# Performance work log

Measured on AMD Instinct MI355X. Metric: run time of the kernel, lower is better.

The kernel has to match this reference:

```python
import jax, jax.numpy as jnp
import numpy as np

N, E = 4096, 40960
NODE_DIM, RADIAL_DIM = 16, 8
M, HD, LAT = 64, 32, 128
NUM_LAYERS = 2
R_MAX, POLY_P, ENV_NORM = 5.0, 6.0, 5.0
ISQRTD = 5.0  # math.isqrt(32) == 5 in the original source


def setup_inputs() -> dict:
    key = jax.random.key(0)
    ks = jax.random.split(key, 20)
    def w(k, shape, fan_in):
        return jax.random.normal(k, shape, jnp.float32) / np.float32(np.sqrt(fan_in))
    return {
        "node_attrs": jax.random.uniform(ks[0], (N, NODE_DIM), jnp.float32),
        "edge_radial": jax.random.normal(ks[1], (E, RADIAL_DIM), jnp.float32),
        "edge_angular": jax.random.normal(ks[2], (E, 4), jnp.float32),
        "edge_lengths": jax.random.uniform(ks[3], (E,), jnp.float32) * (R_MAX * 0.9),
        "edge_index": jax.random.randint(ks[4], (2, E), 0, N),
        "W_lat0": w(ks[5], (2 * NODE_DIM + RADIAL_DIM, LAT), 2 * NODE_DIM + RADIAL_DIM),
        "W_lat1": w(ks[6], (LAT + 2 * M, LAT), LAT + 2 * M),
        "W_final": w(ks[7], (LAT + 2 * M, M), LAT + 2 * M),
        "W_env0": w(ks[8], (LAT, 5 * M), LAT),  # 320 = feat weights(128) + env weights(128) + gate(64)
        "W_env1": w(ks[9], (LAT, 3 * M), LAT),  # 192 = env weights(128) + gate(64)
        "W_q": w(ks[10], (NUM_LAYERS, NODE_DIM, M * HD), NODE_DIM),
        "W_k": w(ks[11], (NUM_LAYERS, M, M * HD), M),
        "W_envlin": w(ks[12], (NUM_LAYERS, 2, M, M), M),
        "W_prod": w(ks[13], (NUM_LAYERS, NODE_DIM, M), NODE_DIM),
        "W_lin_s": w(ks[14], (NUM_LAYERS, 2, M, M), 2 * M),
        "W_lin_v": w(ks[15], (NUM_LAYERS, 3, M, M), 3 * M),
        "alpha": jax.random.normal(ks[16], (NUM_LAYERS,), jnp.float32),
    }


def _poly_cutoff(r):
    # PolynomialCutoff with p=6
    x = r / R_MAX
    p = POLY_P
    c = (1.0 - ((p + 1.0) * (p + 2.0) / 2.0) * x ** p
         + p * (p + 2.0) * x ** (p + 1.0)
         - (p * (p + 1.0) / 2.0) * x ** (p + 2.0))
    return jnp.where(x < 1.0, c, 0.0)


def reference(node_attrs, edge_radial, edge_angular, edge_lengths, edge_index,
              W_lat0, W_lat1, W_final, W_env0, W_env1, W_q, W_k,
              W_envlin, W_prod, W_lin_s, W_lin_v, alpha):
    n_nodes = node_attrs.shape[0]
    center, neigh = edge_index[0], edge_index[1]
    cutoff = _poly_cutoff(edge_lengths)[:, None]  # [E,1]
    sh0 = edge_angular[:, 0:1]                    # [E,1] l=0 SH
    sh1 = edge_angular[:, 1:4]                    # [E,3] l=1 SH

    # two-body latent
    two_body_in = jnp.concatenate([node_attrs[center], node_attrs[neigh], edge_radial], -1)
    latent = jax.nn.silu(two_body_in @ W_lat0) * cutoff  # [E,LAT]

    feat_s = feat_v = None
    for l in range(NUM_LAYERS):
        if l == 0:
            wts = latent @ W_env0
            w_feat = wts[:, :2 * M].reshape(-1, M, 2)
            w_env = wts[:, 2 * M:4 * M].reshape(-1, M, 2)
            w_gate = wts[:, 4 * M:]
            feat_s = w_feat[..., 0] * sh0                         # [E,M]
            feat_v = w_feat[..., 1][..., None] * sh1[:, None, :]  # [E,M,3]
        else:
            wts = latent @ W_env1
            w_env = wts[:, :2 * M].reshape(-1, M, 2)
            w_gate = wts[:, 2 * M:]
        # weighted-channel env embedding of the edge spherical harmonics
        emb_s = w_env[..., 0] * sh0                               # [E,M]
        emb_v = w_env[..., 1][..., None] * sh1[:, None, :]        # [E,M,3]
        # attention-like query/key scalar product per channel
        q = (node_attrs @ W_q[l]).reshape(-1, M, HD)[center]      # [E,M,HD]
        k = ((emb_s * w_gate) @ W_k[l]).reshape(-1, M, HD)        # [E,M,HD]
        attn = jax.nn.sigmoid(jnp.einsum('emd,emd->em', q, k) / ISQRTD)
        g_edge = attn * cutoff                                    # [E,M]
        # neighbor scatter-sum, normalized (env_sum_normalizations buffer = 5.0)
        env_s = jax.ops.segment_sum(emb_s * g_edge, center, num_segments=n_nodes) / ENV_NORM
        env_v = jax.ops.segment_sum(emb_v * g_edge[..., None], center, num_segments=n_nodes) / ENV_NORM
        # env_linear: per-l channel mixing
        env_s = env_s @ W_envlin[l, 0]
        env_v = jnp.einsum('nmc,mk->nkc', env_v, W_envlin[l, 1])
        # element-dependent product-basis gating (simplified EquivariantProductBasisBlock)
        gate_n = node_attrs @ W_prod[l]
        env_s = env_s * gate_n
        env_v = env_v * gate_n[..., None]
        es, ev = env_s[center], env_v[center]
        # channel-wise (uuu) tensor product at lmax=1
        s1 = feat_s * es                                             # 0e x 0e -> 0e
        s2 = jnp.einsum('emc,emc->em', feat_v, ev) / jnp.sqrt(3.0)   # 1o x 1o -> 0e
        v1 = feat_s[..., None] * ev                                  # 0e x 1o -> 1o
        v2 = feat_v * es[..., None]                                  # 1o x 0e -> 1o
        v3 = jnp.cross(feat_v, ev) / jnp.sqrt(2.0)                   # 1o x 1o -> 1o
        scalars = jnp.stack([s1, s2], 1)       # [E,2,M]
        vectors = jnp.stack([v1, v2, v3], 1)   # [E,3,M,3]
        # irreps Linear: path + channel mixing
        feat_s = jnp.einsum('epm,pmk->ek', scalars, W_lin_s[l]) / jnp.sqrt(2.0 * M)
        feat_v = jnp.einsum('epmc,pmk->ekc', vectors, W_lin_v[l]) / jnp.sqrt(3.0 * M)
        sc_flat = scalars.transpose(0, 2, 1).reshape(-1, 2 * M)  # tp scalar outs
        lat_in = jnp.concatenate([latent, sc_flat], -1)
        if l < NUM_LAYERS - 1:
            new_lat = jax.nn.silu(lat_in @ W_lat1) * cutoff
            co = 1.0 / jnp.sqrt(1.0 + alpha[l] ** 2)  # latent resnet update
            latent = co * latent + (alpha[l] * co) * new_lat
        else:
            feat_s = lat_in @ W_final  # final_latent -> out scalar features [E,M]
    # reshape_back_features: concat scalar + vector irrep blocks
    return jnp.concatenate([feat_s, feat_v.reshape(-1, 3 * M)], -1)  # [E, 4*M]
```

## Files before the change

### kernel.cpp

```cpp
#include <hip/hip_runtime.h>

constexpr int Nn  = 4096;
constexpr int Ee  = 40960;
constexpr int ND  = 16;
constexpr int Mm  = 64;
constexpr int HD  = 32;

#define DI __device__ __forceinline__

DI float silu_f(float x) { return x / (1.f + __expf(-x)); }
DI unsigned short bf16r(float f) {
    unsigned u = __float_as_uint(f);
    return (unsigned short)((u + 0x7FFFu + ((u >> 16) & 1u)) >> 16);
}
DI float bf16f(unsigned short h) { return __uint_as_float(((unsigned)h) << 16); }

__global__ void k_zero(float* __restrict__ p, int n) {
    int i = blockIdx.x * 256 + threadIdx.x;
    if (i < n) p[i] = 0.f;
}

__global__ void k_cutoff(const float* __restrict__ len, float* __restrict__ cut) {
    int e = blockIdx.x * 256 + threadIdx.x;
    if (e >= Ee) return;
    float x  = len[e] * 0.2f;
    float x2 = x * x, x4 = x2 * x2, x6 = x4 * x2;
    float c  = 1.f - 28.f * x6 + 48.f * x6 * x - 21.f * x4 * x4;
    cut[e] = (x < 1.f) ? c : 0.f;
}

__global__ void k_qk(const float* __restrict__ Wq, const float* __restrict__ Wk,
                     float* __restrict__ QKT) {
    int idx = blockIdx.x * 256 + threadIdx.x;
    int mp = idx & 63;
    int m  = (idx >> 6) & 63;
    int a  = (idx >> 12) & 15;
    int l  = idx >> 16;
    const float* q = Wq + ((size_t)(l * ND + a)) * 2048 + m * HD;
    const float* k = Wk + ((size_t)(l * Mm + mp)) * 2048 + m * HD;
    float acc = 0.f;
#pragma unroll
    for (int d = 0; d < HD; ++d) acc += q[d] * k[d];
    QKT[(((size_t)l * 16 + a) * 16 + (mp >> 2)) * 256 + m * 4 + (mp & 3)] = acc;
}

__global__ void k_permB(const float* __restrict__ Wls, float* __restrict__ Bp) {
    int idx = blockIdx.x * 256 + threadIdx.x;
    int k = idx & 63, row = idx >> 6;
    int m = row >> 1, pp = row & 1;
    Bp[row * 64 + k] = Wls[pp * 4096 + m * 64 + k];
}

__global__ void k_qw(const float* __restrict__ na, const float* __restrict__ QKT,
                     ushort4* __restrict__ QWh) {
    int n = blockIdx.x >> 2;
    int g = ((blockIdx.x & 3) << 2) + (threadIdx.x >> 6);
    int m = threadIdx.x & 63;
    const float4* QK4 = (const float4*)QKT;
    const float* nar = na + n * ND;
    float4 acc = {0.f, 0.f, 0.f, 0.f};
#pragma unroll
    for (int a = 0; a < ND; ++a) {
        float w = nar[a];
        float4 q = QK4[(a * 16 + g) * 64 + m];
        acc.x += w * q.x; acc.y += w * q.y; acc.z += w * q.z; acc.w += w * q.w;
    }
    ushort4 o;
    o.x = bf16r(acc.x); o.y = bf16r(acc.y); o.z = bf16r(acc.z); o.w = bf16r(acc.w);
    QWh[((size_t)n * 16 + g) * 64 + m] = o;
}

__global__ void k_A2(const float* __restrict__ wts, const float* __restrict__ ang,
                     const float* __restrict__ cut, const int* __restrict__ ctr,
                     const ushort4* __restrict__ QWh,
                     float* __restrict__ env_s, float* __restrict__ env_v) {
    __shared__ float xs[256];
    int wid = threadIdx.x >> 6, m = threadIdx.x & 63;
    int e = blockIdx.x * 4 + wid;
    int c = ctr[e];
    float cute = cut[e];
    float4 sh = ((const float4*)ang)[e];
    const float* w = wts + (size_t)e * 192;
    float2 we = ((const float2*)w)[m];
    float wg = w[128 + m];
    float es_ = we.x * sh.x;
    float ev0 = we.y * sh.y, ev1 = we.y * sh.z, ev2 = we.y * sh.w;
    xs[threadIdx.x] = es_ * wg;
    __syncthreads();
    const float4* xv = (const float4*)(xs + wid * 64);
    const ushort4* qrow = QWh + (size_t)c * 1024;
    float logit = 0.f;
#pragma unroll
    for (int g = 0; g < 16; ++g) {
        ushort4 q = qrow[g * 64 + m];
        float4 x = xv[g];
        logit += bf16f(q.x) * x.x + bf16f(q.y) * x.y + bf16f(q.z) * x.z + bf16f(q.w) * x.w;
    }
    float attn = 1.f / (1.f + __expf(-logit * 0.2f));
    float ga = attn * cute * 0.2f;
    atomicAdd(&env_s[(size_t)c * 64 + m], es_ * ga);
    atomicAdd(&env_v[(size_t)c * 192 + m],       ev0 * ga);
    atomicAdd(&env_v[(size_t)c * 192 + 64 + m],  ev1 * ga);
    atomicAdd(&env_v[(size_t)c * 192 + 128 + m], ev2 * ga);
}

__global__ void k_C_s(const float* __restrict__ fs, const float* __restrict__ fv,
                      const float* __restrict__ es_t, const float* __restrict__ ev_t,
                      const int* __restrict__ ctr, float* __restrict__ sc_mp) {
    int wid = threadIdx.x >> 6, m = threadIdx.x & 63;
    int e = blockIdx.x * 4 + wid;
    int c = ctr[e];
    float es  = es_t[(size_t)c * 64 + m];
    float ev0 = ev_t[(size_t)c * 192 + m];
    float ev1 = ev_t[(size_t)c * 192 + 64 + m];
    float ev2 = ev_t[(size_t)c * 192 + 128 + m];
    float f  = fs[(size_t)e * 64 + m];
    float g0 = fv[(size_t)e * 192 + m];
    float g1 = fv[(size_t)e * 192 + 64 + m];
    float g2 = fv[(size_t)e * 192 + 128 + m];
    float2 sp;
    sp.x = f * es;
    sp.y = (g0 * ev0 + g1 * ev1 + g2 * ev2) * 0.5773502691896258f;
    ((float2*)sc_mp)[(size_t)e * 64 + m] = sp;
}

template <int P>
__global__ void k_C_v(const float* __restrict__ fs, const float* __restrict__ fv,
                      const float* __restrict__ es_t, const float* __restrict__ ev_t,
                      const int* __restrict__ ctr, float* __restrict__ vec) {
    constexpr int Pb = (P + 1) % 3, Pc = (P + 2) % 3;
    int wid = threadIdx.x >> 6, m = threadIdx.x & 63;
    int e = blockIdx.x * 4 + wid;
    int c = ctr[e];
    float es  = es_t[(size_t)c * 64 + m];
    float evP = ev_t[(size_t)c * 192 + P  * 64 + m];
    float evB = ev_t[(size_t)c * 192 + Pb * 64 + m];
    float evC = ev_t[(size_t)c * 192 + Pc * 64 + m];
    float f   = fs[(size_t)e * 64 + m];
    float gP  = fv[(size_t)e * 192 + P  * 64 + m];
    float gB  = fv[(size_t)e * 192 + Pb * 64 + m];
    float gC  = fv[(size_t)e * 192 + Pc * 64 + m];
    constexpr float is2 = 0.7071067811865475f;
    vec[(size_t)e * 192 + m]       = f * evP;
    vec[(size_t)e * 192 + 64 + m]  = gP * es;
    vec[(size_t)e * 192 + 128 + m] = (gB * evC - gC * evB) * is2;
}

__global__ __launch_bounds__(256) void k_gemm(
    const float* __restrict__ A, int lda, const float* __restrict__ A2,
    const int* __restrict__ ctr, const int* __restrict__ ngh,
    const float* __restrict__ naw, const float* __restrict__ er,
    const float* __restrict__ B, int ldb, int K,
    float* __restrict__ C, int ldc, int cstride, float scale,
    const float* __restrict__ cut, const float* __restrict__ oldlat,
    const float* __restrict__ alphap, const float* __restrict__ gate,
    const float* __restrict__ ang, float* __restrict__ fsP, float* __restrict__ fvP,
    int modeA, int modeE) {
    __shared__ float a_s[16][72];
    __shared__ float b_s[16][64];
    int t = threadIdx.x;
    int row0 = blockIdx.x * 64;
    int j0 = blockIdx.y * 64;
    int tx = t & 15, ty = t >> 4;
    int ar = t & 63, akq = t >> 6;
    int bj = (t & 15) * 4, bk = t >> 4;
    float acc[4][4] = {};
    int nchunks = (K + 15) >> 4;
    for (int ch = 0; ch < nchunks; ++ch) {
        int k0 = ch * 16;
        {
            int row = row0 + ar;
            int k = k0 + akq * 4;
            float4 v;
            if (modeA == 0) {
                v = *(const float4*)(A + (size_t)row * lda + k);
            } else if (modeA == 1) {
                const float* src = (k < 128) ? (A + (size_t)row * 128 + k)
                                             : (A2 + (size_t)row * 128 + (k - 128));
                v = *(const float4*)src;
            } else {
                float tmp[4];
#pragma unroll
                for (int i = 0; i < 4; ++i) {
                    int kk = k + i; float val = 0.f;
                    if (kk < 16)      val = naw[(size_t)ctr[row] * 16 + kk];
                    else if (kk < 32) val = naw[(size_t)ngh[row] * 16 + (kk - 16)];
                    else if (kk < 40) val = er[(size_t)row * 8 + (kk - 32)];
                    tmp[i] = val;
                }
                v.x = tmp[0]; v.y = tmp[1]; v.z = tmp[2]; v.w = tmp[3];
            }
            a_s[akq * 4 + 0][ar] = v.x;
            a_s[akq * 4 + 1][ar] = v.y;
            a_s[akq * 4 + 2][ar] = v.z;
            a_s[akq * 4 + 3][ar] = v.w;
        }
        {
            int k = k0 + bk;
            float4 v = {0.f, 0.f, 0.f, 0.f};
            if (k < K) v = *(const float4*)(B + (size_t)k * ldb + j0 + bj);
            *(float4*)&b_s[bk][bj] = v;
        }
        __syncthreads();
#pragma unroll
        for (int k = 0; k < 16; ++k) {
            float4 a4 = *(const float4*)&a_s[k][ty * 4];
            float4 b4 = *(const float4*)&b_s[k][tx * 4];
            acc[0][0] += a4.x * b4.x; acc[0][1] += a4.x * b4.y; acc[0][2] += a4.x * b4.z; acc[0][3] += a4.x * b4.w;
            acc[1][0] += a4.y * b4.x; acc[1][1] += a4.y * b4.y; acc[1][2] += a4.y * b4.z; acc[1][3] += a4.y * b4.w;
            acc[2][0] += a4.z * b4.x; acc[2][1] += a4.z * b4.y; acc[2][2] += a4.z * b4.z; acc[2][3] += a4.z * b4.w;
            acc[3][0] += a4.w * b4.x; acc[3][1] += a4.w * b4.y; acc[3][2] += a4.w * b4.z; acc[3][3] += a4.w * b4.w;
        }
        __syncthreads();
    }
    float a0 = 0.f, co = 1.f;
    if (modeE == 2) { a0 = alphap[0]; co = rsqrtf(1.f + a0 * a0); }
#pragma unroll
    for (int r = 0; r < 4; ++r) {
        int row = row0 + ty * 4 + r;
        if (modeE == 4) {
            float4 sh = ((const float4*)ang)[row];
#pragma unroll
            for (int i = 0; i < 4; ++i) {
                int col = j0 + tx * 4 + i;
                int m = col >> 1;
                float v = acc[r][i];
                if (col & 1) {
                    fvP[(size_t)row * 192 + m]       = v * sh.y;
                    fvP[(size_t)row * 192 + 64 + m]  = v * sh.z;
                    fvP[(size_t)row * 192 + 128 + m] = v * sh.w;
                } else {
                    fsP[(size_t)row * 64 + m] = v * sh.x;
                }
            }
            continue;
        }
        float cu = (modeE == 1 || modeE == 2) ? cut[row] : 0.f;
#pragma unroll
        for (int i = 0; i < 4; ++i) {
            int col = j0 + tx * 4 + i;
            float v;
            if (modeE == 1)      v = silu_f(acc[r][i]) * cu;
            else if (modeE == 2) {
                float nl = silu_f(acc[r][i]) * cu;
                v = co * oldlat[(size_t)row * 128 + col] + a0 * co * nl;
            } else if (modeE == 3) v = acc[r][i] * scale * gate[(size_t)row * 64 + col];
            else                 v = acc[r][i] * scale;
            C[(size_t)row * ldc + (size_t)col * cstride] = v;
        }
    }
}

extern "C" void kernel_launch(void* const* d_in, const int* in_sizes, int n_in,
                              void* d_out, int out_size, void* d_ws, size_t ws_size,
                              hipStream_t stream) {
    const float* na     = (const float*)d_in[0];
    const float* er     = (const float*)d_in[1];
    const float* ang    = (const float*)d_in[2];
    const float* len    = (const float*)d_in[3];
    const int*   ei     = (const int*)d_in[4];
    const float* W_lat0 = (const float*)d_in[5];
    const float* W_lat1 = (const float*)d_in[6];
    const float* W_fin  = (const float*)d_in[7];
    const float* W_env0 = (const float*)d_in[8];
    const float* W_env1 = (const float*)d_in[9];
    const float* W_q    = (const float*)d_in[10];
    const float* W_k    = (const float*)d_in[11];
    const float* W_evl  = (const float*)d_in[12];
    const float* W_prod = (const float*)d_in[13];
    const float* W_ls   = (const float*)d_in[14];
    const float* W_lv   = (const float*)d_in[15];
    const float* alpha  = (const float*)d_in[16];
    float* out = (float*)d_out;

    const int* ctr = ei;
    const int* ngh = ei + Ee;

    float* ws = (float*)d_ws;
    float* wtsv  = ws;
    float* QWreg = wtsv + 7864320;
    float* sc_mp = QWreg;
    float* fvB   = QWreg + 8388608;
    float* lat   = QWreg + 16777216;
    float* lat2  = lat + 5242880;
    float* fs    = lat2 + 5242880;
    float* cut   = fs + 2621440;
    float* QKT   = cut + 40960;
    float* env_s = QKT + 131072;
    float* env_v = env_s + 262144;
    float* es_t  = env_v + 786432;
    float* ev_t  = es_t + 262144;
    float* gateb = ev_t + 786432;
    float* Wlsp  = gateb + 262144;
    float* fvA   = out;

    const float rs128 = 0.08838834764831845f;
    const float rs192 = 0.07216878364870323f;

    k_cutoff<<<(Ee + 255) / 256, 256, 0, stream>>>(len, cut);
    k_qk<<<512, 256, 0, stream>>>(W_q, W_k, QKT);
    k_permB<<<32, 256, 0, stream>>>(W_ls, Wlsp);
    k_gemm<<<dim3(Ee / 64, 2), 256, 0, stream>>>(nullptr, 0, nullptr, ctr, ngh, na, er,
        W_lat0, 128, 40, lat, 128, 1, 1.f, cut, nullptr, nullptr, nullptr, nullptr, nullptr, nullptr, 2, 1);

    for (int l = 0; l < 2; ++l) {
        const float* latin = (l == 0) ? lat : lat2;
        k_qw<<<Nn * 4, 256, 0, stream>>>(na, QKT + (size_t)l * 65536, (ushort4*)QWreg);
        k_zero<<<(Nn * 256 + 255) / 256, 256, 0, stream>>>(env_s, Nn * 256);
        if (l == 0) {
            k_gemm<<<dim3(Ee / 64, 2), 256, 0, stream>>>(latin, 128, nullptr, nullptr, nullptr, nullptr, nullptr,
                W_env0, 320, 128, nullptr, 0, 1, 1.f, nullptr, nullptr, nullptr, nullptr, ang, fs, fvA, 0, 4);
            k_gemm<<<dim3(Ee / 64, 3), 256, 0, stream>>>(latin, 128, nullptr, nullptr, nullptr, nullptr, nullptr,
                W_env0 + 128, 320, 128, wtsv, 192, 1, 1.f, nullptr, nullptr, nullptr, nullptr, nullptr, nullptr, nullptr, 0, 0);
        } else {
            k_gemm<<<dim3(Ee / 64, 3), 256, 0, stream>>>(latin, 128, nullptr, nullptr, nullptr, nullptr, nullptr,
                W_env1, 192, 128, wtsv, 192, 1, 1.f, nullptr, nullptr, nullptr, nullptr, nullptr, nullptr, nullptr, 0, 0);
        }
        k_A2<<<Ee / 4, 256, 0, stream>>>(wtsv, ang, cut, ctr, (const ushort4*)QWreg, env_s, env_v);
        k_gemm<<<dim3(Nn / 64, 1), 256, 0, stream>>>(na, 16, nullptr, nullptr, nullptr, nullptr, nullptr,
            W_prod + (size_t)l * 1024, 64, 16, gateb, 64, 1, 1.f, nullptr, nullptr, nullptr, nullptr, nullptr, nullptr, nullptr, 0, 0);
        k_gemm<<<dim3(Nn / 64, 1), 256, 0, stream>>>(env_s, 64, nullptr, nullptr, nullptr, nullptr, nullptr,
            W_evl + (size_t)l * 8192, 64, 64, es_t, 64, 1, 1.f, nullptr, nullptr, nullptr, gateb, nullptr, nullptr, nullptr, 0, 3);
        for (int c = 0; c < 3; ++c)
            k_gemm<<<dim3(Nn / 64, 1), 256, 0, stream>>>(env_v + c * 64, 192, nullptr, nullptr, nullptr, nullptr, nullptr,
                W_evl + (size_t)l * 8192 + 4096, 64, 64, ev_t + c * 64, 192, 1, 1.f, nullptr, nullptr, nullptr, gateb, nullptr, nullptr, nullptr, 0, 3);
        const float* fvsrc = (l == 0) ? fvA : fvB;
        k_C_s<<<Ee / 4, 256, 0, stream>>>(fs, fvsrc, es_t, ev_t, ctr, sc_mp);
        for (int c = 0; c < 3; ++c) {
            if (c == 0)      k_C_v<0><<<Ee / 4, 256, 0, stream>>>(fs, fvsrc, es_t, ev_t, ctr, wtsv);
            else if (c == 1) k_C_v<1><<<Ee / 4, 256, 0, stream>>>(fs, fvsrc, es_t, ev_t, ctr, wtsv);
            else             k_C_v<2><<<Ee / 4, 256, 0, stream>>>(fs, fvsrc, es_t, ev_t, ctr, wtsv);
            if (l == 0) {
                k_gemm<<<dim3(Ee / 64, 1), 256, 0, stream>>>(wtsv, 192, nullptr, nullptr, nullptr, nullptr, nullptr,
                    W_lv, 64, 192, fvB + c * 64, 192, 1, rs192, nullptr, nullptr, nullptr, nullptr, nullptr, nullptr, nullptr, 0, 0);
            } else {
                k_gemm<<<dim3(Ee / 64, 1), 256, 0, stream>>>(wtsv, 192, nullptr, nullptr, nullptr, nullptr, nullptr,
                    W_lv + 12288, 64, 192, out + 64 + c, 256, 3, rs192, nullptr, nullptr, nullptr, nullptr, nullptr, nullptr, nullptr, 0, 0);
            }
        }
        if (l == 0) {
            k_gemm<<<dim3(Ee / 64, 1), 256, 0, stream>>>(sc_mp, 128, nullptr, nullptr, nullptr, nullptr, nullptr,
                Wlsp, 64, 128, fs, 64, 1, rs128, nullptr, nullptr, nullptr, nullptr, nullptr, nullptr, nullptr, 0, 0);
            k_gemm<<<dim3(Ee / 64, 2), 256, 0, stream>>>(lat, 128, sc_mp, nullptr, nullptr, nullptr, nullptr,
                W_lat1, 128, 256, lat2, 128, 1, 1.f, cut, lat, alpha, nullptr, nullptr, nullptr, nullptr, 1, 2);
        } else {
            k_gemm<<<dim3(Ee / 64, 1), 256, 0, stream>>>(lat2, 128, sc_mp, nullptr, nullptr, nullptr, nullptr,
                W_fin, 64, 256, out, 256, 1, 1.f, nullptr, nullptr, nullptr, nullptr, nullptr, nullptr, nullptr, 1, 0);
        }
    }
    (void)in_sizes; (void)n_in; (void)out_size; (void)ws_size;
}
```

Before: 895.1 us.

## Enlarge GEMM tile to 128 rows with 128 threads and fold k_C_s into k_C_v

The generic GEMM kernel now uses a 128x64 output tile computed by 128 threads, each holding a 2x4x2x4 register block, which raises register-level reuse of the shared-memory operands. All launches are updated to the new grid and block size. Separately, the scalar tensor-product kernel k_C_s is removed and its work is done inside k_C_v<0>, which already loads the same operands, saving one launch and a redundant gather. In exchange the GEMM uses more registers per thread and launches half as many blocks, and the node GEMMs (4096 rows) get only 32 blocks, which may leave the GPU underoccupied.

```diff
diff --git a/kernel.cpp b/kernel.cpp
--- a/kernel.cpp
+++ b/kernel.cpp
@@ -104,30 +104,11 @@
     atomicAdd(&env_v[(size_t)c * 192 + 128 + m], ev2 * ga);
 }
 
-__global__ void k_C_s(const float* __restrict__ fs, const float* __restrict__ fv,
-                      const float* __restrict__ es_t, const float* __restrict__ ev_t,
-                      const int* __restrict__ ctr, float* __restrict__ sc_mp) {
-    int wid = threadIdx.x >> 6, m = threadIdx.x & 63;
-    int e = blockIdx.x * 4 + wid;
-    int c = ctr[e];
-    float es  = es_t[(size_t)c * 64 + m];
-    float ev0 = ev_t[(size_t)c * 192 + m];
-    float ev1 = ev_t[(size_t)c * 192 + 64 + m];
-    float ev2 = ev_t[(size_t)c * 192 + 128 + m];
-    float f  = fs[(size_t)e * 64 + m];
-    float g0 = fv[(size_t)e * 192 + m];
-    float g1 = fv[(size_t)e * 192 + 64 + m];
-    float g2 = fv[(size_t)e * 192 + 128 + m];
-    float2 sp;
-    sp.x = f * es;
-    sp.y = (g0 * ev0 + g1 * ev1 + g2 * ev2) * 0.5773502691896258f;
-    ((float2*)sc_mp)[(size_t)e * 64 + m] = sp;
-}
-
 template <int P>
 __global__ void k_C_v(const float* __restrict__ fs, const float* __restrict__ fv,
                       const float* __restrict__ es_t, const float* __restrict__ ev_t,
-                      const int* __restrict__ ctr, float* __restrict__ vec) {
+                      const int* __restrict__ ctr, float* __restrict__ vec,
+                      float* __restrict__ sc_mp) {
     constexpr int Pb = (P + 1) % 3, Pc = (P + 2) % 3;
     int wid = threadIdx.x >> 6, m = threadIdx.x & 63;
     int e = blockIdx.x * 4 + wid;
@@ -144,9 +125,15 @@
     vec[(size_t)e * 192 + m]       = f * evP;
     vec[(size_t)e * 192 + 64 + m]  = gP * es;
     vec[(size_t)e * 192 + 128 + m] = (gB * evC - gC * evB) * is2;
-}
-
-__global__ __launch_bounds__(256) void k_gemm(
+    if (P == 0) {
+        float2 sp;
+        sp.x = f * es;
+        sp.y = (gP * evP + gB * evB + gC * evC) * 0.5773502691896258f;
+        ((float2*)sc_mp)[(size_t)e * 64 + m] = sp;
+    }
+}
+
+__global__ __launch_bounds__(128) void k_gemm(
     const float* __restrict__ A, int lda, const float* __restrict__ A2,
     const int* __restrict__ ctr, const int* __restrict__ ngh,
     const float* __restrict__ naw, const float* __restrict__ er,
@@ -156,21 +143,24 @@
     const float* __restrict__ alphap, const float* __restrict__ gate,
     const float* __restrict__ ang, float* __restrict__ fsP, float* __restrict__ fvP,
     int modeA, int modeE) {
-    __shared__ float a_s[16][72];
+    __shared__ float a_s[16][132];
     __shared__ float b_s[16][64];
     int t = threadIdx.x;
-    int row0 = blockIdx.x * 64;
+    int row0 = blockIdx.x * 128;
     int j0 = blockIdx.y * 64;
-    int tx = t & 15, ty = t >> 4;
-    int ar = t & 63, akq = t >> 6;
-    int bj = (t & 15) * 4, bk = t >> 4;
-    float acc[4][4] = {};
+    int tx = t & 7, ty = t >> 3;
+    int sar = t >> 2;
+    int sak = (t & 3) * 4;
+    int sbk = t >> 4;
+    int sbn = (t & 15) * 4;
+    float acc[2][4][2][4] = {};
     int nchunks = (K + 15) >> 4;
     for (int ch = 0; ch < nchunks; ++ch) {
         int k0 = ch * 16;
-        {
-            int row = row0 + ar;
-            int k = k0 + akq * 4;
+#pragma unroll
+        for (int p = 0; p < 4; ++p) {
+            int row = row0 + sar + 32 * p;
+            int k = k0 + sak;
             float4 v;
             if (modeA == 0) {
                 v = *(const float4*)(A + (size_t)row * lda + k);
@@ -190,41 +180,57 @@
                 }
                 v.x = tmp[0]; v.y = tmp[1]; v.z = tmp[2]; v.w = tmp[3];
             }
-            a_s[akq * 4 + 0][ar] = v.x;
-            a_s[akq * 4 + 1][ar] = v.y;
-            a_s[akq * 4 + 2][ar] = v.z;
-            a_s[akq * 4 + 3][ar] = v.w;
-        }
-        {
-            int k = k0 + bk;
+            int rr = sar + 32 * p;
+            a_s[sak + 0][rr] = v.x;
+            a_s[sak + 1][rr] = v.y;
+            a_s[sak + 2][rr] = v.z;
+            a_s[sak + 3][rr] = v.w;
+        }
+#pragma unroll
+        for (int q = 0; q < 2; ++q) {
+            int kk = sbk + 8 * q;
+            int k = k0 + kk;
             float4 v = {0.f, 0.f, 0.f, 0.f};
-            if (k < K) v = *(const float4*)(B + (size_t)k * ldb + j0 + bj);
-            *(float4*)&b_s[bk][bj] = v;
+            if (k < K) v = *(const float4*)(B + (size_t)k * ldb + j0 + sbn);
+            *(float4*)&b_s[kk][sbn] = v;
         }
         __syncthreads();
 #pragma unroll
         for (int k = 0; k < 16; ++k) {
-            float4 a4 = *(const float4*)&a_s[k][ty * 4];
-            float4 b4 = *(const float4*)&b_s[k][tx * 4];
-            acc[0][0] += a4.x * b4.x; acc[0][1] += a4.x * b4.y; acc[0][2] += a4.x * b4.z; acc[0][3] += a4.x * b4.w;
-            acc[1][0] += a4.y * b4.x; acc[1][1] += a4.y * b4.y; acc[1][2] += a4.y * b4.z; acc[1][3] += a4.y * b4.w;
-            acc[2][0] += a4.z * b4.x; acc[2][1] += a4.z * b4.y; acc[2][2] += a4.z * b4.z; acc[2][3] += a4.z * b4.w;
-            acc[3][0] += a4.w * b4.x; acc[3][1] += a4.w * b4.y; acc[3][2] += a4.w * b4.z; acc[3][3] += a4.w * b4.w;
+            float4 A0 = *(const float4*)&a_s[k][ty * 4];
+            float4 A1 = *(const float4*)&a_s[k][64 + ty * 4];
+            float4 B0 = *(const float4*)&b_s[k][tx * 4];
+            float4 B1 = *(const float4*)&b_s[k][32 + tx * 4];
+            float av[2][4] = {{A0.x, A0.y, A0.z, A0.w}, {A1.x, A1.y, A1.z, A1.w}};
+            float bv[2][4] = {{B0.x, B0.y, B0.z, B0.w}, {B1.x, B1.y, B1.z, B1.w}};
+#pragma unroll
+            for (int rh = 0; rh < 2; ++rh)
+#pragma unroll
+                for (int r = 0; r < 4; ++r)
+#pragma unroll
+                    for (int ch2 = 0; ch2 < 2; ++ch2)
+#pragma unroll
+                        for (int i = 0; i < 4; ++i)
+                            acc[rh][r][ch2][i] += av[rh][r] * bv[ch2][i];
         }
         __syncthreads();
     }
     float a0 = 0.f, co = 1.f;
     if (modeE == 2) { a0 = alphap[0]; co = rsqrtf(1.f + a0 * a0); }
 #pragma unroll
+    for (int rh = 0; rh < 2; ++rh)
+#pragma unroll
     for (int r = 0; r < 4; ++r) {
-        int row = row0 + ty * 4 + r;
+        int row = row0 + rh * 64 + ty * 4 + r;
         if (modeE == 4) {
             float4 sh = ((const float4*)ang)[row];
 #pragma unroll
+            for (int ch2 = 0; ch2 < 2; ++ch2)
+#pragma unroll
             for (int i = 0; i < 4; ++i) {
-                int col = j0 + tx * 4 + i;
+                int col = j0 + ch2 * 32 + tx * 4 + i;
                 int m = col >> 1;
-                float v = acc[r][i];
+                float v = acc[rh][r][ch2][i];
                 if (col & 1) {
                     fvP[(size_t)row * 192 + m]       = v * sh.y;
                     fvP[(size_t)row * 192 + 64 + m]  = v * sh.z;
@@ -237,15 +243,17 @@
         }
         float cu = (modeE == 1 || modeE == 2) ? cut[row] : 0.f;
 #pragma unroll
+        for (int ch2 = 0; ch2 < 2; ++ch2)
+#pragma unroll
         for (int i = 0; i < 4; ++i) {
-            int col = j0 + tx * 4 + i;
+            int col = j0 + ch2 * 32 + tx * 4 + i;
             float v;
-            if (modeE == 1)      v = silu_f(acc[r][i]) * cu;
+            if (modeE == 1)      v = silu_f(acc[rh][r][ch2][i]) * cu;
             else if (modeE == 2) {
-                float nl = silu_f(acc[r][i]) * cu;
+                float nl = silu_f(acc[rh][r][ch2][i]) * cu;
                 v = co * oldlat[(size_t)row * 128 + col] + a0 * co * nl;
-            } else if (modeE == 3) v = acc[r][i] * scale * gate[(size_t)row * 64 + col];
-            else                 v = acc[r][i] * scale;
+            } else if (modeE == 3) v = acc[rh][r][ch2][i] * scale * gate[(size_t)row * 64 + col];
+            else                 v = acc[rh][r][ch2][i] * scale;
             C[(size_t)row * ldc + (size_t)col * cstride] = v;
         }
     }
@@ -300,7 +308,7 @@
     k_cutoff<<<(Ee + 255) / 256, 256, 0, stream>>>(len, cut);
     k_qk<<<512, 256, 0, stream>>>(W_q, W_k, QKT);
     k_permB<<<32, 256, 0, stream>>>(W_ls, Wlsp);
-    k_gemm<<<dim3(Ee / 64, 2), 256, 0, stream>>>(nullptr, 0, nullptr, ctr, ngh, na, er,
+    k_gemm<<<dim3(Ee / 128, 2), 128, 0, stream>>>(nullptr, 0, nullptr, ctr, ngh, na, er,
         W_lat0, 128, 40, lat, 128, 1, 1.f, cut, nullptr, nullptr, nullptr, nullptr, nullptr, nullptr, 2, 1);
 
     for (int l = 0; l < 2; ++l) {
@@ -308,43 +316,42 @@
         k_qw<<<Nn * 4, 256, 0, stream>>>(na, QKT + (size_t)l * 65536, (ushort4*)QWreg);
         k_zero<<<(Nn * 256 + 255) / 256, 256, 0, stream>>>(env_s, Nn * 256);
         if (l == 0) {
-            k_gemm<<<dim3(Ee / 64, 2), 256, 0, stream>>>(latin, 128, nullptr, nullptr, nullptr, nullptr, nullptr,
+            k_gemm<<<dim3(Ee / 128, 2), 128, 0, stream>>>(latin, 128, nullptr, nullptr, nullptr, nullptr, nullptr,
                 W_env0, 320, 128, nullptr, 0, 1, 1.f, nullptr, nullptr, nullptr, nullptr, ang, fs, fvA, 0, 4);
-            k_gemm<<<dim3(Ee / 64, 3), 256, 0, stream>>>(latin, 128, nullptr, nullptr, nullptr, nullptr, nullptr,
+            k_gemm<<<dim3(Ee / 128, 3), 128, 0, stream>>>(latin, 128, nullptr, nullptr, nullptr, nullptr, nullptr,
                 W_env0 + 128, 320, 128, wtsv, 192, 1, 1.f, nullptr, nullptr, nullptr, nullptr, nullptr, nullptr, nullptr, 0, 0);
         } else {
-            k_gemm<<<dim3(Ee / 64, 3), 256, 0, stream>>>(latin, 128, nullptr, nullptr, nullptr, nullptr, nullptr,
+            k_gemm<<<dim3(Ee / 128, 3), 128, 0, stream>>>(latin, 128, nullptr, nullptr, nullptr, nullptr, nullptr,
                 W_env1, 192, 128, wtsv, 192, 1, 1.f, nullptr, nullptr, nullptr, nullptr, nullptr, nullptr, nullptr, 0, 0);
         }
         k_A2<<<Ee / 4, 256, 0, stream>>>(wtsv, ang, cut, ctr, (const ushort4*)QWreg, env_s, env_v);
-        k_gemm<<<dim3(Nn / 64, 1), 256, 0, stream>>>(na, 16, nullptr, nullptr, nullptr, nullptr, nullptr,
+        k_gemm<<<dim3(Nn / 128, 1), 128, 0, stream>>>(na, 16, nullptr, nullptr, nullptr, nullptr, nullptr,
             W_prod + (size_t)l * 1024, 64, 16, gateb, 64, 1, 1.f, nullptr, nullptr, nullptr, nullptr, nullptr, nullptr, nullptr, 0, 0);
-        k_gemm<<<dim3(Nn / 64, 1), 256, 0, stream>>>(env_s, 64, nullptr, nullptr, nullptr, nullptr, nullptr,
+        k_gemm<<<dim3(Nn / 128, 1), 128, 0, stream>>>(env_s, 64, nullptr, nullptr, nullptr, nullptr, nullptr,
             W_evl + (size_t)l * 8192, 64, 64, es_t, 64, 1, 1.f, nullptr, nullptr, nullptr, gateb, nullptr, nullptr, nullptr, 0, 3);
         for (int c = 0; c < 3; ++c)
-            k_gemm<<<dim3(Nn / 64, 1), 256, 0, stream>>>(env_v + c * 64, 192, nullptr, nullptr, nullptr, nullptr, nullptr,
+            k_gemm<<<dim3(Nn / 128, 1), 128, 0, stream>>>(env_v + c * 64, 192, nullptr, nullptr, nullptr, nullptr, nullptr,
                 W_evl + (size_t)l * 8192 + 4096, 64, 64, ev_t + c * 64, 192, 1, 1.f, nullptr, nullptr, nullptr, gateb, nullptr, nullptr, nullptr, 0, 3);
         const float* fvsrc = (l == 0) ? fvA : fvB;
-        k_C_s<<<Ee / 4, 256, 0, stream>>>(fs, fvsrc, es_t, ev_t, ctr, sc_mp);
         for (int c = 0; c < 3; ++c) {
-            if (c == 0)      k_C_v<0><<<Ee / 4, 256, 0, stream>>>(fs, fvsrc, es_t, ev_t, ctr, wtsv);
-            else if (c == 1) k_C_v<1><<<Ee / 4, 256, 0, stream>>>(fs, fvsrc, es_t, ev_t, ctr, wtsv);
-            else             k_C_v<2><<<Ee / 4, 256, 0, stream>>>(fs, fvsrc, es_t, ev_t, ctr, wtsv);
+            if (c == 0)      k_C_v<0><<<Ee / 4, 256, 0, stream>>>(fs, fvsrc, es_t, ev_t, ctr, wtsv, sc_mp);
+            else if (c == 1) k_C_v<1><<<Ee / 4, 256, 0, stream>>>(fs, fvsrc, es_t, ev_t, ctr, wtsv, sc_mp);
+            else             k_C_v<2><<<Ee / 4, 256, 0, stream>>>(fs, fvsrc, es_t, ev_t, ctr, wtsv, sc_mp);
             if (l == 0) {
-                k_gemm<<<dim3(Ee / 64, 1), 256, 0, stream>>>(wtsv, 192, nullptr, nullptr, nullptr, nullptr, nullptr,
+                k_gemm<<<dim3(Ee / 128, 1), 128, 0, stream>>>(wtsv, 192, nullptr, nullptr, nullptr, nullptr, nullptr,
                     W_lv, 64, 192, fvB + c * 64, 192, 1, rs192, nullptr, nullptr, nullptr, nullptr, nullptr, nullptr, nullptr, 0, 0);
             } else {
-                k_gemm<<<dim3(Ee / 64, 1), 256, 0, stream>>>(wtsv, 192, nullptr, nullptr, nullptr, nullptr, nullptr,
+                k_gemm<<<dim3(Ee / 128, 1), 128, 0, stream>>>(wtsv, 192, nullptr, nullptr, nullptr, nullptr, nullptr,
                     W_lv + 12288, 64, 192, out + 64 + c, 256, 3, rs192, nullptr, nullptr, nullptr, nullptr, nullptr, nullptr, nullptr, 0, 0);
             }
         }
         if (l == 0) {
-            k_gemm<<<dim3(Ee / 64, 1), 256, 0, stream>>>(sc_mp, 128, nullptr, nullptr, nullptr, nullptr, nullptr,
+            k_gemm<<<dim3(Ee / 128, 1), 128, 0, stream>>>(sc_mp, 128, nullptr, nullptr, nullptr, nullptr, nullptr,
                 Wlsp, 64, 128, fs, 64, 1, rs128, nullptr, nullptr, nullptr, nullptr, nullptr, nullptr, nullptr, 0, 0);
-            k_gemm<<<dim3(Ee / 64, 2), 256, 0, stream>>>(lat, 128, sc_mp, nullptr, nullptr, nullptr, nullptr,
+            k_gemm<<<dim3(Ee / 128, 2), 128, 0, stream>>>(lat, 128, sc_mp, nullptr, nullptr, nullptr, nullptr,
                 W_lat1, 128, 256, lat2, 128, 1, 1.f, cut, lat, alpha, nullptr, nullptr, nullptr, nullptr, 1, 2);
         } else {
-            k_gemm<<<dim3(Ee / 64, 1), 256, 0, stream>>>(lat2, 128, sc_mp, nullptr, nullptr, nullptr, nullptr,
+            k_gemm<<<dim3(Ee / 128, 1), 128, 0, stream>>>(lat2, 128, sc_mp, nullptr, nullptr, nullptr, nullptr,
                 W_fin, 64, 256, out, 256, 1, 1.f, nullptr, nullptr, nullptr, nullptr, nullptr, nullptr, nullptr, 1, 0);
         }
     }
```

New measurement: 1.279 ms. +42.9%, slower.
